# Kernel tuning notes

Measured on AMD Instinct MI355X. Metric: run time of the kernel, lower is better.

## Reference

```python
import math
import jax, jax.numpy as jnp
import numpy as np

DIM = 4096
N_HEADS = 32
N_KV_HEADS = 8
HEAD_DIM = DIM // N_HEADS  # 128
N_REP = N_HEADS // N_KV_HEADS  # 4
BSZ = 1
SEQLEN = 2048
ROPE_THETA = 500000.0


def setup_inputs() -> dict:
    key = jax.random.key(0)
    ks = jax.random.split(key, 8)
    s = 1.0 / math.sqrt(DIM)
    x = jax.random.normal(ks[0], (BSZ, SEQLEN, DIM), dtype=jnp.float32)
    wq = jax.random.normal(ks[1], (DIM, N_HEADS * HEAD_DIM), dtype=jnp.float32) * s
    wk = jax.random.normal(ks[2], (DIM, N_KV_HEADS * HEAD_DIM), dtype=jnp.float32) * s
    wv = jax.random.normal(ks[3], (DIM, N_KV_HEADS * HEAD_DIM), dtype=jnp.float32) * s
    wo = jax.random.normal(ks[4], (N_HEADS * HEAD_DIM, DIM), dtype=jnp.float32) * s
    # RoPE frequencies: freqs_cis[t, j] = exp(i * t * theta^{-2j/hd})
    inv_freq = 1.0 / (ROPE_THETA ** (jnp.arange(0, HEAD_DIM, 2, dtype=jnp.float32) / HEAD_DIM))
    t = jnp.arange(SEQLEN, dtype=jnp.float32)
    angles = jnp.outer(t, inv_freq)  # [S, hd/2]
    freqs_cos = jnp.cos(angles)
    freqs_sin = jnp.sin(angles)
    # causal additive mask [S, S]: 0 on/below diagonal, -inf above
    mask = jnp.triu(jnp.full((SEQLEN, SEQLEN), float('-inf'), dtype=jnp.float32), k=1)
    cache_k = jnp.zeros((BSZ, SEQLEN, N_KV_HEADS, HEAD_DIM), dtype=jnp.float32)
    cache_v = jnp.zeros((BSZ, SEQLEN, N_KV_HEADS, HEAD_DIM), dtype=jnp.float32)
    return {"x": x, "wq": wq, "wk": wk, "wv": wv, "wo": wo,
            "freqs_cos": freqs_cos, "freqs_sin": freqs_sin, "mask": mask,
            "cache_k": cache_k, "cache_v": cache_v, "start_pos": 0}


def _apply_rotary(xq, xk, cos, sin):
    # xq: [B,S,Hq,hd], xk: [B,S,Hkv,hd]; cos/sin: [S, hd/2]
    def rot(x):
        b, s, h, d = x.shape
        xr = x.reshape(b, s, h, d // 2, 2)
        a, bb = xr[..., 0], xr[..., 1]
        c = cos[None, :, None, :]
        sn = sin[None, :, None, :]
        out = jnp.stack([a * c - bb * sn, a * sn + bb * c], axis=-1)
        return out.reshape(b, s, h, d)
    return rot(xq), rot(xk)


def reference(x, wq, wk, wv, wo, freqs_cos, freqs_sin, mask, cache_k, cache_v, start_pos):
    bsz, seqlen, _ = x.shape
    xq = (x @ wq).reshape(bsz, seqlen, N_HEADS, HEAD_DIM)
    xk = (x @ wk).reshape(bsz, seqlen, N_KV_HEADS, HEAD_DIM)
    xv = (x @ wv).reshape(bsz, seqlen, N_KV_HEADS, HEAD_DIM)
    xq, xk = _apply_rotary(xq, xk, freqs_cos, freqs_sin)
    # KV-cache append
    cache_k = jax.lax.dynamic_update_slice(cache_k, xk, (0, start_pos, 0, 0))
    cache_v = jax.lax.dynamic_update_slice(cache_v, xv, (0, start_pos, 0, 0))
    kv_len = start_pos + seqlen
    keys = cache_k[:, :kv_len]    # [B, T, Hkv, hd]
    values = cache_v[:, :kv_len]
    # GQA repeat (logical; einsum reshaping keeps math identical)
    keys = jnp.repeat(keys, N_REP, axis=2)      # [B, T, Hq, hd]
    values = jnp.repeat(values, N_REP, axis=2)
    scale = 1.0 / math.sqrt(HEAD_DIM)
    scores = jnp.einsum('bqhd,bkhd->bhqk', xq, keys) * scale
    scores = scores + mask[None, None, :, :kv_len]
    probs = jax.nn.softmax(scores.astype(jnp.float32), axis=-1).astype(xq.dtype)
    out = jnp.einsum('bhqk,bkhd->bqhd', probs, values)
    out = out.reshape(bsz, seqlen, N_HEADS * HEAD_DIM)
    return out @ wo
```

## Files before the change

kernel.cpp:

```cpp
#include <hip/hip_runtime.h>
#include <hip/hip_bf16.h>

typedef unsigned short u16;
typedef short short8 __attribute__((ext_vector_type(8)));
typedef float floatx4 __attribute__((ext_vector_type(4)));

#define DIM 4096
#define SEQ 2048
#define NH 32
#define NKV 8
#define HD 128
#define QKV_N 6144

static __device__ __forceinline__ float b2f(u16 u) {
    return __uint_as_float(((unsigned int)u) << 16);
}
static __device__ __forceinline__ u16 f2b(float f) {
    unsigned int u = __float_as_uint(f);
    u = (u + 0x7FFFu + ((u >> 16) & 1u)) >> 16;
    return (u16)u;
}
static __device__ __forceinline__ void async16(const u16* g, u16* l) {
    __builtin_amdgcn_global_load_lds((const __attribute__((address_space(1))) void*)g,
                                     (__attribute__((address_space(3))) void*)l, 16, 0, 0);
}

static __device__ __forceinline__ void trans64(const float* __restrict__ src,
                                               u16* __restrict__ dst,
                                               int R, int C, int bx, int by,
                                               int tid, u16* lds ) {
    int c0 = bx * 64, r0 = by * 64;
#pragma unroll
    for (int i = 0; i < 4; i++) {
        int g = i * 256 + tid;
        int r = g >> 4, c4 = g & 15;
        float4 f = *(const float4*)(src + (size_t)(r0 + r) * C + c0 + c4 * 4);
        u16* p = lds + (c4 * 4) * 68 + r;
        p[0]       = f2b(f.x);
        p[68]      = f2b(f.y);
        p[136]     = f2b(f.z);
        p[204]     = f2b(f.w);
    }
    __syncthreads();
#pragma unroll
    for (int i = 0; i < 4; i++) {
        int g = i * 256 + tid;
        int c = g >> 4, rg = g & 15;
        ushort4 v = *(const ushort4*)(lds + c * 68 + rg * 4);
        *(ushort4*)(dst + (size_t)(c0 + c) * R + r0 + rg * 4) = v;
    }
}

__global__ __launch_bounds__(256) void prep_all(const float* __restrict__ wq,
                                                const float* __restrict__ wk,
                                                const float* __restrict__ wv,
                                                const float* __restrict__ wo,
                                                const float* __restrict__ x,
                                                u16* __restrict__ WT,
                                                u16* __restrict__ WOT,
                                                u16* __restrict__ xbf) {
    __shared__ u16 lds[64 * 68];
    int b = blockIdx.x, tid = threadIdx.x;
    if (b < 4096) {
        trans64(wq, WT, 4096, 4096, b & 63, b >> 6, tid, lds);
    } else if (b < 5120) {
        int bb = b - 4096;
        trans64(wk, WT + (size_t)4096 * 4096, 4096, 1024, bb & 15, bb >> 4, tid, lds);
    } else if (b < 6144) {
        int bb = b - 5120;
        trans64(wv, WT + (size_t)5120 * 4096, 4096, 1024, bb & 15, bb >> 4, tid, lds);
    } else if (b < 14336) {
        int i = ((b - 6144) * 256 + tid) * 4;
        float4 f = *(const float4*)(x + i);
        ushort4 o;
        o.x = f2b(f.x); o.y = f2b(f.y); o.z = f2b(f.z); o.w = f2b(f.w);
        *(ushort4*)(xbf + i) = o;
    } else {
        int bb = b - 14336;
        trans64(wo, WOT, 4096, 4096, bb & 63, bb >> 6, tid, lds);
    }
}

__global__ __launch_bounds__(256) void transpose_f32_bf16(const float* __restrict__ src,
                                                          u16* __restrict__ dst,
                                                          int R, int C) {
    __shared__ u16 lds[64 * 68];
    trans64(src, dst, R, C, blockIdx.x, blockIdx.y, threadIdx.x, lds);
}

__global__ __launch_bounds__(256) void rope_tv(u16* __restrict__ X,
                                               const float* __restrict__ fc,
                                               const float* __restrict__ fs,
                                               u16* __restrict__ VT) {
    __shared__ u16 tile[32][33];
    int b = blockIdx.x, tid = threadIdx.x;
    if (b < 20480) {
        int idx = b * 256 + tid;
        int i = idx & 63;
        int rem = idx >> 6;
        int h = rem % 40;
        int pos = rem / 40;
        int col = (h < 32) ? (h * 128 + 2 * i) : (4096 + (h - 32) * 128 + 2 * i);
        size_t off = (size_t)pos * QKV_N + col;
        unsigned int pr = *(unsigned int*)&X[off];
        float a = b2f((u16)(pr & 0xffffu));
        float bb = b2f((u16)(pr >> 16));
        float c = fc[pos * 64 + i];
        float s = fs[pos * 64 + i];
        float na = a * c - bb * s;
        float nb = a * s + bb * c;
        unsigned int outw = ((unsigned int)f2b(nb) << 16) | (unsigned int)f2b(na);
        *(unsigned int*)&X[off] = outw;
    } else {
        int bb = b - 20480;
        int k0 = (bb & 63) * 32, d0 = ((bb >> 6) & 3) * 32, h = bb >> 8;
        const u16* src = X + DIM + NKV * HD + h * HD;
        int xx = tid & 31, y0 = tid >> 5;
#pragma unroll
        for (int i = 0; i < 4; i++) {
            int r = y0 + i * 8;
            tile[r][xx] = src[(size_t)(k0 + r) * QKV_N + d0 + xx];
        }
        __syncthreads();
        u16* dst = VT + ((size_t)h * HD + d0) * SEQ + k0;
#pragma unroll
        for (int i = 0; i < 4; i++) {
            int r = y0 + i * 8;
            dst[(size_t)r * SEQ + xx] = tile[xx][r];
        }
    }
}

template<int MTW, int NTW, bool CF32>
__global__ __launch_bounds__(512, 2) void gemm_pipe(const u16* __restrict__ A,
                                                    const u16* __restrict__ Bt,
                                                    void* __restrict__ Cv,
                                                    int M, int N, int K) {
    constexpr int BM = 32 * MTW;
    constexpr int BN = 64 * NTW;
    constexpr int TILE = (BM + BN) * 32;
    constexpr int ACALLS = BM / 128;
    constexpr int BCALLS = BN / 128;
    constexpr int LPP = ACALLS + BCALLS;

    __shared__ __align__(128) u16 lds[4 * TILE];

    int tid = threadIdx.x;
    int wave = tid >> 6, lane = tid & 63, quad = lane >> 4, l16 = lane & 15;
    int wm = wave >> 2, wn = wave & 3;

    int nwg = gridDim.x;
    int MT = M / BM;
    int orig = blockIdx.x;
    int q = nwg >> 3, r = nwg & 7;
    int xcd = orig & 7, idx = orig >> 3;
    int wg = (xcd < r ? xcd * (q + 1) : r * (q + 1) + (xcd - r) * q) + idx;
    int m0 = (wg % MT) * BM, n0 = (wg / MT) * BN;

    int srow = lane >> 2;
    int g = (lane & 3) ^ ((lane >> 3) & 3);
    const u16* Ap = A + (size_t)(m0 + wave * (BM / 8) + srow) * K + g * 8;
    const u16* Bp = Bt + (size_t)(n0 + wave * (BN / 8) + srow) * K + g * 8;
    int sA = (quad ^ ((l16 >> 1) & 3)) * 8;

    floatx4 acc[MTW][NTW];
#pragma unroll
    for (int i = 0; i < MTW; i++)
#pragma unroll
        for (int j = 0; j < NTW; j++) acc[i][j] = (floatx4){0.f, 0.f, 0.f, 0.f};

    auto stage = [&](int t) {
        int buf = t & 3;
        const u16* a0 = Ap + (size_t)t * 32;
        const u16* b0 = Bp + (size_t)t * 32;
        u16* as = lds + buf * TILE + wave * ((BM / 8) * 32);
        u16* bs = lds + buf * TILE + BM * 32 + wave * ((BN / 8) * 32);
#pragma unroll
        for (int c = 0; c < ACALLS; c++)
            async16(a0 + (size_t)(c * 16) * K, as + c * 512);
#pragma unroll
        for (int c = 0; c < BCALLS; c++)
            async16(b0 + (size_t)(c * 16) * K, bs + c * 512);
    };

    auto compute = [&](int t) {
        int buf = t & 3;
        const u16* Ab = lds + buf * TILE;
        const u16* Bb = Ab + BM * 32;
        short8 a[MTW], b[NTW];
#pragma unroll
        for (int mt = 0; mt < MTW; mt++)
            a[mt] = *(const short8*)&Ab[(wm * (MTW * 16) + mt * 16 + l16) * 32 + sA];
#pragma unroll
        for (int nt = 0; nt < NTW; nt++)
            b[nt] = *(const short8*)&Bb[(wn * (NTW * 16) + nt * 16 + l16) * 32 + sA];
        __builtin_amdgcn_s_setprio(1);
#pragma unroll
        for (int mt = 0; mt < MTW; mt++)
#pragma unroll
            for (int nt = 0; nt < NTW; nt++)
                acc[mt][nt] = __builtin_amdgcn_mfma_f32_16x16x32_bf16(a[mt], b[nt], acc[mt][nt], 0, 0, 0);
        __builtin_amdgcn_s_setprio(0);
    };

    int nk = K >> 5;
    stage(0); stage(1); stage(2);
    asm volatile("s_waitcnt vmcnt(%0)" :: "n"(2 * LPP) : "memory");
    __builtin_amdgcn_s_barrier();
    for (int t = 0; t < nk - 3; t++) {
        stage(t + 3);
        compute(t);
        asm volatile("s_waitcnt vmcnt(%0)" :: "n"(2 * LPP) : "memory");
        __builtin_amdgcn_s_barrier();
    }
    compute(nk - 3);
    asm volatile("s_waitcnt vmcnt(%0)" :: "n"(LPP) : "memory");
    __builtin_amdgcn_s_barrier();
    compute(nk - 2);
    asm volatile("s_waitcnt vmcnt(0)" ::: "memory");
    __builtin_amdgcn_s_barrier();
    compute(nk - 1);

#pragma unroll
    for (int mt = 0; mt < MTW; mt++)
#pragma unroll
        for (int nt = 0; nt < NTW; nt++) {
            int row = m0 + wm * (MTW * 16) + mt * 16 + quad * 4;
            int col = n0 + wn * (NTW * 16) + nt * 16 + l16;
#pragma unroll
            for (int rr = 0; rr < 4; rr++) {
                if constexpr (CF32)
                    ((float*)Cv)[(size_t)(row + rr) * N + col] = acc[mt][nt][rr];
                else
                    ((u16*)Cv)[(size_t)(row + rr) * N + col] = f2b(acc[mt][nt][rr]);
            }
        }
}

__global__ __launch_bounds__(256) void attn_kernel(const u16* __restrict__ Xqkv,
                                                   const u16* __restrict__ VT,
                                                   u16* __restrict__ O) {
    __shared__ u16 Ks[2][64 * 128];
    __shared__ u16 Vt[2][128 * 64];
    __shared__ u16 Ps[4 * 1024];
    int head = blockIdx.y;
    int kvh = head >> 2;
    const u16* Xq = Xqkv + head * HD;
    const u16* Xk = Xqkv + DIM + kvh * HD;
    const u16* Vg = VT + (size_t)kvh * HD * SEQ;
    int tid = threadIdx.x, wave = tid >> 6, lane = tid & 63, quad = lane >> 4, l16 = lane & 15;

    size_t offKe = (size_t)quad * QKV_N + (size_t)((l16 ^ quad) * 8);
    size_t offKo = (size_t)quad * QKV_N + (size_t)((l16 ^ (quad + 4)) * 8);
    size_t offV  = (size_t)(lane >> 3) * SEQ + (size_t)((((lane & 7) ^ ((lane >> 3) & 7))) * 8);
    int sK[4];
#pragma unroll
    for (int ks = 0; ks < 4; ks++) sK[ks] = (ks * 4 + quad) ^ (l16 & 7);

    const float scale = 0.08838834764831845f;

    auto stageKV = [&](int kb, int b) {
#pragma unroll
        for (int c = 0; c < 4; c++) {
            int kc = wave * 4 + c;
            const u16* gp = Xk + (size_t)(kb * 64 + kc * 4) * QKV_N + ((kc & 1) ? offKo : offKe);
            async16(gp, &Ks[b][kc * 512]);
        }
#pragma unroll
        for (int c = 0; c < 4; c++) {
            int vc = wave * 4 + c;
            async16(Vg + (size_t)(vc * 8) * SEQ + (size_t)(kb * 64) + offV, &Vt[b][vc * 512]);
        }
    };

    for (int pass = 0; pass < 2; pass++) {
        int qb = pass ? (31 - blockIdx.x) : blockIdx.x;
        int q0 = qb * 64;

        short8 aq[4];
        {
            const u16* qp = Xq + (size_t)(q0 + wave * 16 + l16) * QKV_N + quad * 8;
#pragma unroll
            for (int ks = 0; ks < 4; ks++) aq[ks] = *(const short8*)(qp + ks * 32);
        }
        float l_i[4] = {0.f, 0.f, 0.f, 0.f};
        floatx4 o_acc[8];
#pragma unroll
        for (int i = 0; i < 8; i++) o_acc[i] = (floatx4){0.f, 0.f, 0.f, 0.f};

        stageKV(0, 0);
        asm volatile("s_waitcnt vmcnt(0)" ::: "memory");
        __builtin_amdgcn_s_barrier();

        int buf = 0;
        for (int kb = 0; kb <= qb; kb++) {
            if (kb < qb) stageKV(kb + 1, buf ^ 1);

            floatx4 s[4];
#pragma unroll
            for (int nt = 0; nt < 4; nt++) s[nt] = (floatx4){0.f, 0.f, 0.f, 0.f};
            __builtin_amdgcn_s_setprio(1);
#pragma unroll
            for (int ks = 0; ks < 4; ks++) {
#pragma unroll
                for (int nt = 0; nt < 4; nt++) {
                    short8 bk = *(const short8*)&Ks[buf][(nt * 16 + l16) * 128 + sK[ks] * 8];
                    s[nt] = __builtin_amdgcn_mfma_f32_16x16x32_bf16(aq[ks], bk, s[nt], 0, 0, 0);
                }
            }
            __builtin_amdgcn_s_setprio(0);

            bool diag = (kb == qb);
            int qrel = wave * 16 + quad * 4;
            float rowsum[4] = {0.f, 0.f, 0.f, 0.f};
#pragma unroll
            for (int nt = 0; nt < 4; nt++) {
                int kcol = nt * 16 + l16;
#pragma unroll
                for (int r = 0; r < 4; r++) {
                    float v = s[nt][r] * scale;
                    if (diag && kcol > qrel + r) v = -__builtin_inff();
                    float p = __expf(fminf(v, 60.f));
                    s[nt][r] = p;
                    rowsum[r] += p;
                }
            }
#pragma unroll
            for (int m = 1; m < 16; m <<= 1)
#pragma unroll
                for (int r = 0; r < 4; r++)
                    rowsum[r] += __shfl_xor(rowsum[r], m);
#pragma unroll
            for (int r = 0; r < 4; r++) l_i[r] += rowsum[r];

            u16* pw = &Ps[wave * 1024];
#pragma unroll
            for (int nt = 0; nt < 4; nt++) {
                int gbase = nt * 2 + (l16 >> 3);
#pragma unroll
                for (int r = 0; r < 4; r++) {
                    int row = quad * 4 + r;
                    int slot = gbase ^ (row & 7);
                    unsigned u = __float_as_uint(s[nt][r]);
                    pw[row * 64 + slot * 8 + (l16 & 7)] = (u16)((u + 0x8000u) >> 16);
                }
            }

            __builtin_amdgcn_s_setprio(1);
#pragma unroll
            for (int ks = 0; ks < 2; ks++) {
                short8 ap = *(const short8*)&Ps[wave * 1024 + l16 * 64 + sK[ks] * 8];
#pragma unroll
                for (int nt = 0; nt < 8; nt++) {
                    short8 bv = *(const short8*)&Vt[buf][(nt * 16 + l16) * 64 + sK[ks] * 8];
                    o_acc[nt] = __builtin_amdgcn_mfma_f32_16x16x32_bf16(ap, bv, o_acc[nt], 0, 0, 0);
                }
            }
            __builtin_amdgcn_s_setprio(0);

            asm volatile("s_waitcnt vmcnt(0)" ::: "memory");
            __builtin_amdgcn_s_barrier();
            buf ^= 1;
        }

        float invl[4];
#pragma unroll
        for (int r = 0; r < 4; r++) invl[r] = 1.f / l_i[r];
#pragma unroll
        for (int nt = 0; nt < 8; nt++) {
            int row = q0 + wave * 16 + quad * 4;
            int col = head * HD + nt * 16 + l16;
#pragma unroll
            for (int r = 0; r < 4; r++)
                O[(size_t)(row + r) * DIM + col] = f2b(o_acc[nt][r] * invl[r]);
        }
    }
}

extern "C" void kernel_launch(void* const* d_in, const int* in_sizes, int n_in,
                              void* d_out, int out_size, void* d_ws, size_t ws_size,
                              hipStream_t stream) {
    const float* x  = (const float*)d_in[0];
    const float* wq = (const float*)d_in[1];
    const float* wk = (const float*)d_in[2];
    const float* wv = (const float*)d_in[3];
    const float* wo = (const float*)d_in[4];
    const float* fc = (const float*)d_in[5];
    const float* fs = (const float*)d_in[6];

    u16* WT   = (u16*)d_ws;
    u16* Xqkv = WT + (size_t)QKV_N * DIM;
    u16* Obuf = Xqkv + (size_t)SEQ * QKV_N;
    u16* xbf  = Obuf;
    u16* VT   = WT + (size_t)5120 * DIM;
    u16* WOT  = Obuf + (size_t)SEQ * DIM;
    float* outp = (float*)d_out;

    size_t base_need = ((size_t)QKV_N * DIM + (size_t)SEQ * QKV_N + (size_t)SEQ * DIM) * sizeof(u16);
    bool bigws = ws_size >= base_need + (size_t)DIM * DIM * sizeof(u16);

    prep_all<<<dim3(bigws ? 18432 : 14336), 256, 0, stream>>>(wq, wk, wv, wo, x, WT, WOT, xbf);

    gemm_pipe<4, 6, false><<<dim3(256), 512, 0, stream>>>(xbf, WT, Xqkv, SEQ, QKV_N, DIM);

    rope_tv<<<dim3(22528), 256, 0, stream>>>(Xqkv, fc, fs, VT);

    attn_kernel<<<dim3(16, NH), 256, 0, stream>>>(Xqkv, VT, Obuf);

    if (!bigws)
        transpose_f32_bf16<<<dim3(64, 64), 256, 0, stream>>>(wo, WT, 4096, 4096);

    gemm_pipe<4, 4, true><<<dim3(256), 512, 0, stream>>>(Obuf, bigws ? WOT : WT, outp, SEQ, DIM, DIM);
}
```

Before: 492.9 us.

## Split GEMM main loop into two ping-pong phases interleaving loads with MFMA

Each main-loop iteration of the pipelined GEMM now runs in two halves. Each half loads part of the B fragments from LDS, issues half of the async global-to-LDS copies for the next stage, and then runs the MFMAs for half of the N tiles. Extra workgroup barriers and sched_barriers fence the phases, so memory issue and matrix math from different waves can interleave. The cost is more barriers per iteration and tighter compiler scheduling constraints, which may add stalls.

```diff
diff --git a/kernel.cpp b/kernel.cpp
--- a/kernel.cpp
+++ b/kernel.cpp
@@ -142,6 +142,8 @@
     constexpr int ACALLS = BM / 128;
     constexpr int BCALLS = BN / 128;
     constexpr int LPP = ACALLS + BCALLS;
+    constexpr int NH2 = NTW / 2;
+    constexpr int SP0 = (LPP + 1) / 2;
 
     __shared__ __align__(128) u16 lds[4 * TILE];
 
@@ -183,6 +185,24 @@
             async16(b0 + (size_t)(c * 16) * K, bs + c * 512);
     };
 
+    auto stagePart = [&](int t, int clo, int chi) {
+        int buf = t & 3;
+        const u16* a0 = Ap + (size_t)t * 32;
+        const u16* b0 = Bp + (size_t)t * 32;
+        u16* as = lds + buf * TILE + wave * ((BM / 8) * 32);
+        u16* bs = lds + buf * TILE + BM * 32 + wave * ((BN / 8) * 32);
+#pragma unroll
+        for (int c = 0; c < LPP; c++) {
+            if (c < clo || c >= chi) continue;
+            if (c < ACALLS) {
+                async16(a0 + (size_t)(c * 16) * K, as + c * 512);
+            } else {
+                int cb = c - ACALLS;
+                async16(b0 + (size_t)(cb * 16) * K, bs + cb * 512);
+            }
+        }
+    };
+
     auto compute = [&](int t) {
         int buf = t & 3;
         const u16* Ab = lds + buf * TILE;
@@ -208,9 +228,44 @@
     asm volatile("s_waitcnt vmcnt(%0)" :: "n"(2 * LPP) : "memory");
     __builtin_amdgcn_s_barrier();
     for (int t = 0; t < nk - 3; t++) {
-        stage(t + 3);
-        compute(t);
+        int buf = t & 3;
+        const u16* Ab = lds + buf * TILE;
+        const u16* Bb = Ab + BM * 32;
+        short8 a[MTW], b0r[NH2];
+#pragma unroll
+        for (int mt = 0; mt < MTW; mt++)
+            a[mt] = *(const short8*)&Ab[(wm * (MTW * 16) + mt * 16 + l16) * 32 + sA];
+#pragma unroll
+        for (int nt = 0; nt < NH2; nt++)
+            b0r[nt] = *(const short8*)&Bb[(wn * (NTW * 16) + nt * 16 + l16) * 32 + sA];
+        stagePart(t + 3, 0, SP0);
+        __builtin_amdgcn_s_barrier();
+        asm volatile("s_waitcnt lgkmcnt(0)" ::: "memory");
+        __builtin_amdgcn_sched_barrier(0);
+        __builtin_amdgcn_s_setprio(1);
+#pragma unroll
+        for (int mt = 0; mt < MTW; mt++)
+#pragma unroll
+            for (int nt = 0; nt < NH2; nt++)
+                acc[mt][nt] = __builtin_amdgcn_mfma_f32_16x16x32_bf16(a[mt], b0r[nt], acc[mt][nt], 0, 0, 0);
+        __builtin_amdgcn_s_setprio(0);
+        __builtin_amdgcn_s_barrier();
+        short8 b1r[NTW - NH2];
+#pragma unroll
+        for (int nt = 0; nt < NTW - NH2; nt++)
+            b1r[nt] = *(const short8*)&Bb[(wn * (NTW * 16) + (NH2 + nt) * 16 + l16) * 32 + sA];
+        stagePart(t + 3, SP0, LPP);
         asm volatile("s_waitcnt vmcnt(%0)" :: "n"(2 * LPP) : "memory");
+        __builtin_amdgcn_s_barrier();
+        asm volatile("s_waitcnt lgkmcnt(0)" ::: "memory");
+        __builtin_amdgcn_sched_barrier(0);
+        __builtin_amdgcn_s_setprio(1);
+#pragma unroll
+        for (int mt = 0; mt < MTW; mt++)
+#pragma unroll
+            for (int nt = 0; nt < NTW - NH2; nt++)
+                acc[mt][NH2 + nt] = __builtin_amdgcn_mfma_f32_16x16x32_bf16(a[mt], b1r[nt], acc[mt][NH2 + nt], 0, 0, 0);
+        __builtin_amdgcn_s_setprio(0);
         __builtin_amdgcn_s_barrier();
     }
     compute(nk - 3);
```

Measured after the change: 489.0 us. No clear change (-0.8%).
